# Kernel optimization log

Measured on AMD Instinct MI355X. Metric: run time of the kernel, lower is better.

The kernel has to match this reference:

```python
import jax, jax.numpy as jnp
import numpy as np

EPS = 1e-6  # torch.nn.PairwiseDistance default eps: dist = ||x - y + eps||_2


def setup_inputs() -> dict:
    key = jax.random.key(0)
    k1, k2 = jax.random.split(key)
    samples = jax.random.normal(k1, (4096, 128), dtype=jnp.float32)   # batch of observations
    V = jax.random.uniform(k2, (65536, 128), dtype=jnp.float32)       # grown node codebook (torch.rand init)
    return {"samples": samples, "V": V}


def reference(samples, V):
    # activate_bmu, vectorized over the batch.
    # torch PairwiseDistance(p=2): d_n = || x - V_n + eps ||_2
    D = samples.shape[-1]
    x_sq = jnp.sum(samples * samples, axis=-1)        # [B]
    v_sq = jnp.sum(V * V, axis=-1)                    # [N]
    xv = jnp.einsum('bd,nd->bn', samples, V)          # [B, N]
    x_sum = jnp.sum(samples, axis=-1)                 # [B]
    v_sum = jnp.sum(V, axis=-1)                       # [N]
    sq = (x_sq[:, None] + v_sq[None, :] - 2.0 * xv
          + 2.0 * EPS * (x_sum[:, None] - v_sum[None, :]) + D * EPS * EPS)
    dists = jnp.sqrt(jnp.maximum(sq, 0.0))            # [B, N]
    # top-2 smallest distances -> BMU b, second BMU s
    neg_top2, idx = jax.lax.top_k(-dists, 2)          # [B, 2]
    b = idx[:, 0]
    s = idx[:, 1]
    a = jnp.exp(neg_top2[:, 0])                       # exp(-b_dist)
    return (b, s, a)
```

## Files before the change

kernel.cpp:

```cpp
#include <hip/hip_runtime.h>
#include <math.h>

#define NS 4096
#define NV 65536
#define DDIM 128
#define EPSV 1e-6f
#define NCHUNK 16
#define TILES_PER_CHUNK 32
#define NTILE 512
#define FLTMAX 3.402823466e+38f
#define IMAX 0x7fffffff

#define XSQ_F    0
#define XSUM_F   4096
#define PART_F   8192
#define D12_F    270336
#define T12_I    278528
#define CELL1_I  286720
#define CELL2_I  290816
#define WS_TILED_BYTE 1605632
#define TILE_BYTES 65536
#define TILE_STRIDE 66560

typedef __attribute__((ext_vector_type(8)))  __bf16        bf16x8;
typedef __attribute__((ext_vector_type(8)))  unsigned short ush8;
typedef __attribute__((ext_vector_type(4)))  unsigned short ush4;
typedef __attribute__((ext_vector_type(16))) float          f32x16;

typedef const __attribute__((address_space(1))) unsigned int* gp_t;
typedef __attribute__((address_space(3))) unsigned int*       lp_t;

__device__ __forceinline__ void async_cp16(const void* g, void* l) {
    __builtin_amdgcn_global_load_lds((gp_t)g, (lp_t)l, 16, 0, 0);
}

__device__ __forceinline__ unsigned short f2bf(float x) {
    unsigned u = __builtin_bit_cast(unsigned, x);
    u += 0x7FFFu + ((u >> 16) & 1u);
    return (unsigned short)(u >> 16);
}
__device__ __forceinline__ float bf2f(unsigned short h) {
    unsigned u = ((unsigned)h) << 16;
    return __builtin_bit_cast(float, u);
}

__device__ __forceinline__ void merge2t(float& d1, int& i1, float& d2, int& i2,
                                        float d, int i) {
    bool b1 = (d < d1) || (d == d1 && i < i1);
    bool b2 = (d < d2) || (d == d2 && i < i2);
    if (b1) { d2 = d1; i2 = i1; d1 = d; i1 = i; }
    else if (b2) { d2 = d; i2 = i; }
}

__device__ __forceinline__ void load_bfrag(const float* __restrict__ samples,
                                           int srow, int q, ush8* bh, ush8* bl) {
    const float4* s4 = (const float4*)samples;
    #pragma unroll
    for (int s = 0; s < 8; s++) {
        float4 x0 = s4[(size_t)srow * 32 + s * 4 + q * 2];
        float4 x1 = s4[(size_t)srow * 32 + s * 4 + q * 2 + 1];
        float xs[8] = {x0.x, x0.y, x0.z, x0.w, x1.x, x1.y, x1.z, x1.w};
        #pragma unroll
        for (int j = 0; j < 8; j++) {
            float y = -2.0f * xs[j];
            unsigned short hh = f2bf(y);
            bh[s][j] = hh;
            bl[s][j] = f2bf(y - bf2f(hh));
        }
    }
}

__device__ __forceinline__ void tile_mfma(const char* __restrict__ base,
                                          const ush8* bh, const ush8* bl,
                                          int q, int l31, f32x16 acc[4]) {
    #pragma unroll
    for (int mi = 0; mi < 4; mi++) {
        const char* cjb = base + TILE_BYTES + (size_t)(mi * 32 + 4 * q) * 4;
        float4 c0 = *(const float4*)(cjb);
        float4 c1 = *(const float4*)(cjb + 32);
        float4 c2 = *(const float4*)(cjb + 64);
        float4 c3 = *(const float4*)(cjb + 96);
        acc[mi][0] = c0.x;  acc[mi][1] = c0.y;  acc[mi][2] = c0.z;  acc[mi][3] = c0.w;
        acc[mi][4] = c1.x;  acc[mi][5] = c1.y;  acc[mi][6] = c1.z;  acc[mi][7] = c1.w;
        acc[mi][8] = c2.x;  acc[mi][9] = c2.y;  acc[mi][10] = c2.z; acc[mi][11] = c2.w;
        acc[mi][12] = c3.x; acc[mi][13] = c3.y; acc[mi][14] = c3.z; acc[mi][15] = c3.w;
    }
    #pragma unroll
    for (int s = 0; s < 8; s++) {
        bf16x8 bhs = __builtin_bit_cast(bf16x8, bh[s]);
        bf16x8 bls = __builtin_bit_cast(bf16x8, bl[s]);
        #pragma unroll
        for (int mi = 0; mi < 4; mi++) {
            bf16x8 ah = *(const bf16x8*)(base + (size_t)((((s * 2 + 0) * 2 + q) * 128) + mi * 32 + l31) * 16);
            bf16x8 al = *(const bf16x8*)(base + (size_t)((((s * 2 + 1) * 2 + q) * 128) + mi * 32 + l31) * 16);
            acc[mi] = __builtin_amdgcn_mfma_f32_32x32x16_bf16(ah, bhs, acc[mi], 0, 0, 0);
            acc[mi] = __builtin_amdgcn_mfma_f32_32x32x16_bf16(ah, bls, acc[mi], 0, 0, 0);
            acc[mi] = __builtin_amdgcn_mfma_f32_32x32x16_bf16(al, bhs, acc[mi], 0, 0, 0);
        }
    }
}

__global__ void vq_prep(const float* __restrict__ samples,
                        const float* __restrict__ V,
                        char* __restrict__ ws) {
    __shared__ float tf[128 * 132];
    float* ws_f = (float*)ws;
    const int b = blockIdx.x;
    const int tid = threadIdx.x;
    if (b >= NV / 128) {
        int row = (b - NV / 128) * 4 + (tid >> 6);
        int lane = tid & 63;
        float2 v = ((const float2*)(samples + (size_t)row * DDIM))[lane];
        float s = v.x + v.y;
        float q = v.x * v.x + v.y * v.y;
        #pragma unroll
        for (int off = 32; off >= 1; off >>= 1) {
            s += __shfl_xor(s, off);
            q += __shfl_xor(q, off);
        }
        if (lane == 0) { ws_f[XSQ_F + row] = q; ws_f[XSUM_F + row] = s; }
        return;
    }
    const int tile = b;
    char* dst = ws + WS_TILED_BYTE + (size_t)tile * TILE_STRIDE;
    const float4* v4 = (const float4*)V;
    #pragma unroll
    for (int i = 0; i < 16; i++) {
        int flat = i * 256 + tid;
        int row = flat >> 5;
        int c4 = flat & 31;
        float4 g = v4[(size_t)(tile * 128 + row) * 32 + c4];
        *(float4*)&tf[row * 132 + c4 * 4] = g;
        float s = g.x + g.y + g.z + g.w;
        float q2 = g.x * g.x + g.y * g.y + g.z * g.z + g.w * g.w;
        #pragma unroll
        for (int off = 16; off >= 1; off >>= 1) {
            s += __shfl_xor(s, off);
            q2 += __shfl_xor(q2, off);
        }
        if ((tid & 31) == 0)
            *(float*)(dst + TILE_BYTES + row * 4) = q2 - 2.0f * EPSV * s;
    }
    __syncthreads();
    #pragma unroll
    for (int i = 0; i < 8; i++) {
        int task = i * 256 + tid;
        int row = task & 127;
        int sq = task >> 7;
        int s = sq >> 1, q = sq & 1;
        float4 lo = *(const float4*)&tf[row * 132 + s * 16 + q * 8];
        float4 hi = *(const float4*)&tf[row * 132 + s * 16 + q * 8 + 4];
        float xs[8] = {lo.x, lo.y, lo.z, lo.w, hi.x, hi.y, hi.z, hi.w};
        ush8 h, l;
        #pragma unroll
        for (int j = 0; j < 8; j++) {
            unsigned short hh = f2bf(xs[j]);
            h[j] = hh;
            l[j] = f2bf(xs[j] - bf2f(hh));
        }
        *(ush8*)(dst + (size_t)((((s * 2 + 0) * 2 + q) * 128) + row) * 16) = h;
        *(ush8*)(dst + (size_t)((((s * 2 + 1) * 2 + q) * 128) + row) * 16) = l;
    }
}

__device__ __forceinline__ void stage_tile512(const char* src, char* l, int tid) {
    #pragma unroll
    for (int i = 0; i < 8; i++) {
        int off = (i * 512 + tid) * 16;
        async_cp16(src + off, l + off);
    }
    if (tid < 64) {
        int off = TILE_BYTES + tid * 16;
        async_cp16(src + off, l + off);
    }
}

__global__ __launch_bounds__(512, 2)
void vq_gemm_topk(const float* __restrict__ samples, char* __restrict__ ws) {
    __shared__ __align__(16) char lds[2][TILE_STRIDE];
    const int tid = threadIdx.x;
    const int w = tid >> 6, lane = tid & 63;
    const int l31 = lane & 31, qb = lane >> 5;
    const int bid = blockIdx.x;
    const int g = bid >> 3;
    const int chunk = (bid & 7) * 2 + (g >> 4);
    const int st = g & 15;
    const int nrow = st * 256 + w * 32 + l31;

    const char* vbase = ws + WS_TILED_BYTE;
    const int tbase = chunk * TILES_PER_CHUNK;

    stage_tile512(vbase + (size_t)tbase * TILE_STRIDE, lds[0], tid);
    ush8 bh[8], bl[8];
    load_bfrag(samples, nrow, qb, bh, bl);
    __syncthreads();

    float D1 = FLTMAX, D2 = FLTMAX;
    int T1 = IMAX, T2 = IMAX;

    #pragma unroll 1
    for (int it = 0; it < TILES_PER_CHUNK; it++) {
        const int cur = it & 1;
        if (it + 1 < TILES_PER_CHUNK)
            stage_tile512(vbase + (size_t)(tbase + it + 1) * TILE_STRIDE,
                          lds[cur ^ 1], tid);
        f32x16 acc[4];
        tile_mfma(lds[cur], bh, bl, qb, l31, acc);
        float t1[4], t2[4];
        #pragma unroll
        for (int mi = 0; mi < 4; mi++) {
            t1[mi] = FLTMAX; t2[mi] = FLTMAX;
            #pragma unroll
            for (int r = 0; r < 16; r++) {
                float v = acc[mi][r];
                t2[mi] = fminf(t2[mi], fmaxf(t1[mi], v));
                t1[mi] = fminf(t1[mi], v);
            }
        }
        float tt1 = t1[0], tt2 = t2[0];
        #pragma unroll
        for (int mi = 1; mi < 4; mi++) {
            float tmp = fmaxf(tt1, t1[mi]);
            tt1 = fminf(tt1, t1[mi]);
            tt2 = fminf(fminf(tmp, tt2), t2[mi]);
        }
        const int tile = tbase + it;
        bool c1 = tt1 < D1;
        float m1 = fminf(D1, tt2);
        float m2 = fminf(D2, tt1);
        int T2a = (tt2 < D1) ? tile : T1;
        int T2b = (tt1 < D2) ? tile : T2;
        D2 = c1 ? m1 : m2;
        T2 = c1 ? T2a : T2b;
        T1 = c1 ? tile : T1;
        D1 = c1 ? tt1 : D1;
        __syncthreads();
    }

    {
        float od1 = __shfl_xor(D1, 32), od2 = __shfl_xor(D2, 32);
        int   ot1 = __shfl_xor(T1, 32), ot2 = __shfl_xor(T2, 32);
        merge2t(D1, T1, D2, T2, od1, ot1);
        merge2t(D1, T1, D2, T2, od2, ot2);
    }
    if (qb == 0) {
        float4* part = (float4*)((float*)ws + PART_F);
        part[(size_t)nrow * NCHUNK + chunk] =
            make_float4(D1, D2, (float)T1, (float)T2);
    }
}

__global__ void vq_merge(float* __restrict__ ws_f, float* __restrict__ out) {
    const int m = blockIdx.x * 256 + threadIdx.x;
    int* ws_i = (int*)ws_f;
    const float4* part = (const float4*)(ws_f + PART_F);
    float d1 = FLTMAX, d2 = FLTMAX;
    int t1 = IMAX, t2 = IMAX;
    #pragma unroll
    for (int c = 0; c < NCHUNK; c++) {
        float4 p = part[(size_t)m * NCHUNK + c];
        merge2t(d1, t1, d2, t2, p.x, (int)p.z);
        merge2t(d1, t1, d2, t2, p.y, (int)p.w);
    }
    ((float2*)(ws_f + D12_F))[m] = make_float2(d1, d2);
    ((int2*)(ws_i + T12_I))[m] = make_int2(t1, t2);
    ws_i[CELL1_I + m] = IMAX;
    ws_i[CELL2_I + m] = IMAX;
    float ci = ws_f[XSQ_F + m] + 2.0f * EPSV * ws_f[XSUM_F + m] + (float)DDIM * EPSV * EPSV;
    out[2 * NS + m] = expf(-sqrtf(fmaxf(ci + d1, 0.0f)));
}

__global__ __launch_bounds__(256)
void vq_recover(const float* __restrict__ samples, char* __restrict__ ws) {
    __shared__ int list[NS];
    __shared__ int lcnt;
    const int tid = threadIdx.x;
    const int w = tid >> 6, lane = tid & 63;
    const int l31 = lane & 31, qb = lane >> 5;
    const int tile = blockIdx.x;
    int* ws_i = (int*)ws;
    float* ws_f = (float*)ws;

    if (tid == 0) lcnt = 0;
    __syncthreads();
    const int2* t12 = (const int2*)(ws_i + T12_I);
    for (int i = tid; i < NS; i += 256) {
        int2 t = t12[i];
        if (t.x == tile || t.y == tile) {
            int p = atomicAdd(&lcnt, 1);
            list[p] = i;
        }
    }
    __syncthreads();
    const int cnt = lcnt;
    if (cnt == 0) return;

    const char* tsrc = ws + WS_TILED_BYTE + (size_t)tile * TILE_STRIDE;
    const float2* d12 = (const float2*)(ws_f + D12_F);
    const float nanf_ = __int_as_float(0x7fc00000);

    for (int b0 = 0; b0 < cnt; b0 += 128) {
        int li = b0 + w * 32 + l31;
        bool valid = li < cnt;
        int m = valid ? list[li] : 0;
        ush8 bh[8], bl[8];
        load_bfrag(samples, m, qb, bh, bl);
        float d1t = nanf_, d2t = nanf_;
        if (valid) {
            float2 dt = d12[m];
            d1t = dt.x; d2t = dt.y;
        }
        f32x16 acc[4];
        tile_mfma(tsrc, bh, bl, qb, l31, acc);
        #pragma unroll
        for (int mi = 0; mi < 4; mi++) {
            #pragma unroll
            for (int r = 0; r < 16; r++) {
                float v = acc[mi][r];
                int idx = tile * 128 + mi * 32 + (r & 3) + 8 * (r >> 2) + 4 * qb;
                if (v == d1t) {
                    int old = atomicMin(&ws_i[CELL1_I + m], idx);
                    int loser = old > idx ? old : idx;
                    atomicMin(&ws_i[CELL2_I + m], loser);
                } else if (v == d2t) {
                    atomicMin(&ws_i[CELL2_I + m], idx);
                }
            }
        }
    }
}

__global__ void vq_finalize(const char* __restrict__ ws, float* __restrict__ out) {
    const int m = blockIdx.x * 256 + threadIdx.x;
    const int* ws_i = (const int*)ws;
    out[m]      = (float)ws_i[CELL1_I + m];
    out[NS + m] = (float)ws_i[CELL2_I + m];
}

extern "C" void kernel_launch(void* const* d_in, const int* in_sizes, int n_in,
                              void* d_out, int out_size, void* d_ws, size_t ws_size,
                              hipStream_t stream) {
    (void)in_sizes; (void)n_in; (void)out_size; (void)ws_size;
    const float* samples = (const float*)d_in[0];
    const float* V = (const float*)d_in[1];
    float* out = (float*)d_out;
    float* ws_f = (float*)d_ws;
    char*  ws_b = (char*)d_ws;

    vq_prep<<<dim3(NV / 128 + NS / 4), 256, 0, stream>>>(samples, V, ws_b);
    vq_gemm_topk<<<dim3((NS / 256) * NCHUNK), 512, 0, stream>>>(samples, ws_b);
    vq_merge<<<dim3(NS / 256), 256, 0, stream>>>(ws_f, out);
    vq_recover<<<dim3(NTILE), 256, 0, stream>>>(samples, ws_b);
    vq_finalize<<<dim3(NS / 256), 256, 0, stream>>>(ws_b, out);
}
```

Before: 300.5 us.

## Keep sample fragments in LDS and stream V tiles from global per warp

The GEMM+top-k kernel now stages a 128-sample block (converted to split bf16) in LDS once, instead of double-buffering codebook tiles in LDS. Each warp reads its own 32-row slice of the V tile directly from global memory and computes two 32x32 accumulators. Partial top-2 results are reduced across warps through LDS before being written out. The grid doubles to cover 128-sample blocks, and the second-smallest update uses fmed3. The recover kernel now async-copies its tile into LDS up front, overlapping that copy with list building. Risks: global-load latency in the main loop is no longer hidden by a prefetch, and the V tile is re-read by more blocks.

```diff
diff --git a/kernel.cpp b/kernel.cpp
--- a/kernel.cpp
+++ b/kernel.cpp
@@ -68,6 +68,24 @@
             bl[s][j] = f2bf(y - bf2f(hh));
         }
     }
+}
+
+__device__ __forceinline__ void cvt_sample_piece(const float4* __restrict__ s4,
+                                                 int srcrow, int row, int kq,
+                                                 char* lds) {
+    float4 xv = s4[(size_t)srcrow * 32 + kq];
+    int k0 = kq * 4, sI = k0 >> 4, qI = (k0 >> 3) & 1, j0 = k0 & 7;
+    float xs[4] = {xv.x, xv.y, xv.z, xv.w};
+    ush4 h, l;
+    #pragma unroll
+    for (int e = 0; e < 4; e++) {
+        float y = -2.0f * xs[e];
+        unsigned short hh = f2bf(y);
+        h[e] = hh;
+        l[e] = f2bf(y - bf2f(hh));
+    }
+    *(ush4*)(lds + ((((sI * 2 + 0) * 2 + qI) * 128) + row) * 16 + j0 * 2) = h;
+    *(ush4*)(lds + ((((sI * 2 + 1) * 2 + qI) * 128) + row) * 16 + j0 * 2) = l;
 }
 
 __device__ __forceinline__ void tile_mfma(const char* __restrict__ base,
@@ -163,90 +181,149 @@
     }
 }
 
-__device__ __forceinline__ void stage_tile512(const char* src, char* l, int tid) {
-    #pragma unroll
-    for (int i = 0; i < 8; i++) {
-        int off = (i * 512 + tid) * 16;
-        async_cp16(src + off, l + off);
-    }
-    if (tid < 64) {
-        int off = TILE_BYTES + tid * 16;
-        async_cp16(src + off, l + off);
-    }
-}
-
 __global__ __launch_bounds__(512, 2)
 void vq_gemm_topk(const float* __restrict__ samples, char* __restrict__ ws) {
-    __shared__ __align__(16) char lds[2][TILE_STRIDE];
+    __shared__ __align__(16) char lds[TILE_BYTES];
     const int tid = threadIdx.x;
     const int w = tid >> 6, lane = tid & 63;
     const int l31 = lane & 31, qb = lane >> 5;
+    const int mi_own = w & 3;
+    const int sh = w >> 2;
     const int bid = blockIdx.x;
     const int g = bid >> 3;
-    const int chunk = (bid & 7) * 2 + (g >> 4);
-    const int st = g & 15;
-    const int nrow = st * 256 + w * 32 + l31;
+    const int chunk = (bid & 7) * 2 + (g >> 5);
+    const int st = g & 31;
+
+    const float4* s4 = (const float4*)samples;
+    #pragma unroll
+    for (int i = 0; i < 8; i++) {
+        int flat = i * 512 + tid;
+        int row = flat >> 5, kq = flat & 31;
+        cvt_sample_piece(s4, st * 128 + row, row, kq, lds);
+    }
+    __syncthreads();
 
     const char* vbase = ws + WS_TILED_BYTE;
     const int tbase = chunk * TILES_PER_CHUNK;
 
-    stage_tile512(vbase + (size_t)tbase * TILE_STRIDE, lds[0], tid);
-    ush8 bh[8], bl[8];
-    load_bfrag(samples, nrow, qb, bh, bl);
-    __syncthreads();
-
-    float D1 = FLTMAX, D2 = FLTMAX;
-    int T1 = IMAX, T2 = IMAX;
+    float D1a = FLTMAX, D2a = FLTMAX, D1b = FLTMAX, D2b = FLTMAX;
+    int T1a = IMAX, T2a = IMAX, T1b = IMAX, T2b = IMAX;
 
     #pragma unroll 1
     for (int it = 0; it < TILES_PER_CHUNK; it++) {
-        const int cur = it & 1;
-        if (it + 1 < TILES_PER_CHUNK)
-            stage_tile512(vbase + (size_t)(tbase + it + 1) * TILE_STRIDE,
-                          lds[cur ^ 1], tid);
-        f32x16 acc[4];
-        tile_mfma(lds[cur], bh, bl, qb, l31, acc);
-        float t1[4], t2[4];
-        #pragma unroll
-        for (int mi = 0; mi < 4; mi++) {
-            t1[mi] = FLTMAX; t2[mi] = FLTMAX;
+        const int tile = tbase + it;
+        const char* tsrc = vbase + (size_t)tile * TILE_STRIDE;
+        const char* cjb = tsrc + TILE_BYTES + (size_t)(mi_own * 32 + 4 * qb) * 4;
+        float4 c0 = *(const float4*)(cjb);
+        float4 c1 = *(const float4*)(cjb + 32);
+        float4 c2 = *(const float4*)(cjb + 64);
+        float4 c3 = *(const float4*)(cjb + 96);
+        f32x16 acc0, acc1;
+        acc0[0] = c0.x;  acc0[1] = c0.y;  acc0[2] = c0.z;  acc0[3] = c0.w;
+        acc0[4] = c1.x;  acc0[5] = c1.y;  acc0[6] = c1.z;  acc0[7] = c1.w;
+        acc0[8] = c2.x;  acc0[9] = c2.y;  acc0[10] = c2.z; acc0[11] = c2.w;
+        acc0[12] = c3.x; acc0[13] = c3.y; acc0[14] = c3.z; acc0[15] = c3.w;
+        acc1 = acc0;
+        #pragma unroll
+        for (int hs = 0; hs < 2; hs++) {
+            ush8 ah[4], al[4];
+            #pragma unroll
+            for (int si = 0; si < 4; si++) {
+                int s = hs * 4 + si;
+                ah[si] = *(const ush8*)(tsrc + (size_t)((((s * 2 + 0) * 2 + qb) * 128) + mi_own * 32 + l31) * 16);
+                al[si] = *(const ush8*)(tsrc + (size_t)((((s * 2 + 1) * 2 + qb) * 128) + mi_own * 32 + l31) * 16);
+            }
+            #pragma unroll
+            for (int si = 0; si < 4; si++) {
+                int s = hs * 4 + si;
+                bf16x8 a_h = __builtin_bit_cast(bf16x8, ah[si]);
+                bf16x8 a_l = __builtin_bit_cast(bf16x8, al[si]);
+                bf16x8 b0h = *(const bf16x8*)(lds + (size_t)((((s * 2 + 0) * 2 + qb) * 128) + sh * 64 + l31) * 16);
+                bf16x8 b0l = *(const bf16x8*)(lds + (size_t)((((s * 2 + 1) * 2 + qb) * 128) + sh * 64 + l31) * 16);
+                bf16x8 b1h = *(const bf16x8*)(lds + (size_t)((((s * 2 + 0) * 2 + qb) * 128) + sh * 64 + 32 + l31) * 16);
+                bf16x8 b1l = *(const bf16x8*)(lds + (size_t)((((s * 2 + 1) * 2 + qb) * 128) + sh * 64 + 32 + l31) * 16);
+                acc0 = __builtin_amdgcn_mfma_f32_32x32x16_bf16(a_h, b0h, acc0, 0, 0, 0);
+                acc0 = __builtin_amdgcn_mfma_f32_32x32x16_bf16(a_h, b0l, acc0, 0, 0, 0);
+                acc0 = __builtin_amdgcn_mfma_f32_32x32x16_bf16(a_l, b0h, acc0, 0, 0, 0);
+                acc1 = __builtin_amdgcn_mfma_f32_32x32x16_bf16(a_h, b1h, acc1, 0, 0, 0);
+                acc1 = __builtin_amdgcn_mfma_f32_32x32x16_bf16(a_h, b1l, acc1, 0, 0, 0);
+                acc1 = __builtin_amdgcn_mfma_f32_32x32x16_bf16(a_l, b1h, acc1, 0, 0, 0);
+            }
+        }
+        {
+            float t1 = FLTMAX, t2 = FLTMAX;
             #pragma unroll
             for (int r = 0; r < 16; r++) {
-                float v = acc[mi][r];
-                t2[mi] = fminf(t2[mi], fmaxf(t1[mi], v));
-                t1[mi] = fminf(t1[mi], v);
-            }
-        }
-        float tt1 = t1[0], tt2 = t2[0];
-        #pragma unroll
-        for (int mi = 1; mi < 4; mi++) {
-            float tmp = fmaxf(tt1, t1[mi]);
-            tt1 = fminf(tt1, t1[mi]);
-            tt2 = fminf(fminf(tmp, tt2), t2[mi]);
-        }
-        const int tile = tbase + it;
-        bool c1 = tt1 < D1;
-        float m1 = fminf(D1, tt2);
-        float m2 = fminf(D2, tt1);
-        int T2a = (tt2 < D1) ? tile : T1;
-        int T2b = (tt1 < D2) ? tile : T2;
-        D2 = c1 ? m1 : m2;
-        T2 = c1 ? T2a : T2b;
-        T1 = c1 ? tile : T1;
-        D1 = c1 ? tt1 : D1;
-        __syncthreads();
+                float v = acc0[r];
+                t2 = __builtin_amdgcn_fmed3f(t1, t2, v);
+                t1 = fminf(t1, v);
+            }
+            bool c1 = t1 < D1a;
+            float m1 = fminf(D1a, t2);
+            float m2 = fminf(D2a, t1);
+            int T2x = (t2 < D1a) ? tile : T1a;
+            int T2y = (t1 < D2a) ? tile : T2a;
+            D2a = c1 ? m1 : m2;
+            T2a = c1 ? T2x : T2y;
+            T1a = c1 ? tile : T1a;
+            D1a = c1 ? t1 : D1a;
+        }
+        {
+            float t1 = FLTMAX, t2 = FLTMAX;
+            #pragma unroll
+            for (int r = 0; r < 16; r++) {
+                float v = acc1[r];
+                t2 = __builtin_amdgcn_fmed3f(t1, t2, v);
+                t1 = fminf(t1, v);
+            }
+            bool c1 = t1 < D1b;
+            float m1 = fminf(D1b, t2);
+            float m2 = fminf(D2b, t1);
+            int T2x = (t2 < D1b) ? tile : T1b;
+            int T2y = (t1 < D2b) ? tile : T2b;
+            D2b = c1 ? m1 : m2;
+            T2b = c1 ? T2x : T2y;
+            T1b = c1 ? tile : T1b;
+            D1b = c1 ? t1 : D1b;
+        }
     }
 
     {
-        float od1 = __shfl_xor(D1, 32), od2 = __shfl_xor(D2, 32);
-        int   ot1 = __shfl_xor(T1, 32), ot2 = __shfl_xor(T2, 32);
-        merge2t(D1, T1, D2, T2, od1, ot1);
-        merge2t(D1, T1, D2, T2, od2, ot2);
-    }
+        float od1 = __shfl_xor(D1a, 32), od2 = __shfl_xor(D2a, 32);
+        int   ot1 = __shfl_xor(T1a, 32), ot2 = __shfl_xor(T2a, 32);
+        merge2t(D1a, T1a, D2a, T2a, od1, ot1);
+        merge2t(D1a, T1a, D2a, T2a, od2, ot2);
+    }
+    {
+        float od1 = __shfl_xor(D1b, 32), od2 = __shfl_xor(D2b, 32);
+        int   ot1 = __shfl_xor(T1b, 32), ot2 = __shfl_xor(T2b, 32);
+        merge2t(D1b, T1b, D2b, T2b, od1, ot1);
+        merge2t(D1b, T1b, D2b, T2b, od2, ot2);
+    }
+    __syncthreads();
+    float4* scratch = (float4*)lds;
     if (qb == 0) {
+        scratch[mi_own * 128 + sh * 64 + l31]      = make_float4(D1a, D2a, (float)T1a, (float)T2a);
+        scratch[mi_own * 128 + sh * 64 + 32 + l31] = make_float4(D1b, D2b, (float)T1b, (float)T2b);
+    }
+    __syncthreads();
+    if (mi_own == 0 && qb == 0) {
         float4* part = (float4*)((float*)ws + PART_F);
-        part[(size_t)nrow * NCHUNK + chunk] =
-            make_float4(D1, D2, (float)T1, (float)T2);
+        #pragma unroll
+        for (int gg = 0; gg < 2; gg++) {
+            int sidx = sh * 64 + gg * 32 + l31;
+            float4 p0 = scratch[sidx];
+            float d1 = p0.x, d2 = p0.y;
+            int t1 = (int)p0.z, t2 = (int)p0.w;
+            #pragma unroll
+            for (int mm = 1; mm < 4; mm++) {
+                float4 p = scratch[mm * 128 + sidx];
+                merge2t(d1, t1, d2, t2, p.x, (int)p.z);
+                merge2t(d1, t1, d2, t2, p.y, (int)p.w);
+            }
+            part[(size_t)(st * 128 + sidx) * NCHUNK + chunk] =
+                make_float4(d1, d2, (float)t1, (float)t2);
+        }
     }
 }
 
@@ -272,6 +349,7 @@
 
 __global__ __launch_bounds__(256)
 void vq_recover(const float* __restrict__ samples, char* __restrict__ ws) {
+    __shared__ __align__(16) char sbuf[TILE_STRIDE];
     __shared__ int list[NS];
     __shared__ int lcnt;
     const int tid = threadIdx.x;
@@ -281,6 +359,16 @@
     int* ws_i = (int*)ws;
     float* ws_f = (float*)ws;
 
+    const char* tsrc = ws + WS_TILED_BYTE + (size_t)tile * TILE_STRIDE;
+    #pragma unroll
+    for (int i = 0; i < 16; i++) {
+        int off = (i * 256 + tid) * 16;
+        async_cp16(tsrc + off, sbuf + off);
+    }
+    if (tid < 64) {
+        int off = TILE_BYTES + tid * 16;
+        async_cp16(tsrc + off, sbuf + off);
+    }
     if (tid == 0) lcnt = 0;
     __syncthreads();
     const int2* t12 = (const int2*)(ws_i + T12_I);
@@ -295,7 +383,6 @@
     const int cnt = lcnt;
     if (cnt == 0) return;
 
-    const char* tsrc = ws + WS_TILED_BYTE + (size_t)tile * TILE_STRIDE;
     const float2* d12 = (const float2*)(ws_f + D12_F);
     const float nanf_ = __int_as_float(0x7fc00000);
 
@@ -311,7 +398,7 @@
             d1t = dt.x; d2t = dt.y;
         }
         f32x16 acc[4];
-        tile_mfma(tsrc, bh, bl, qb, l31, acc);
+        tile_mfma(sbuf, bh, bl, qb, l31, acc);
         #pragma unroll
         for (int mi = 0; mi < 4; mi++) {
             #pragma unroll
@@ -348,7 +435,7 @@
     char*  ws_b = (char*)d_ws;
 
     vq_prep<<<dim3(NV / 128 + NS / 4), 256, 0, stream>>>(samples, V, ws_b);
-    vq_gemm_topk<<<dim3((NS / 256) * NCHUNK), 512, 0, stream>>>(samples, ws_b);
+    vq_gemm_topk<<<dim3((NS / 128) * NCHUNK), 512, 0, stream>>>(samples, ws_b);
     vq_merge<<<dim3(NS / 256), 256, 0, stream>>>(ws_f, out);
     vq_recover<<<dim3(NTILE), 256, 0, stream>>>(samples, ws_b);
     vq_finalize<<<dim3(NS / 256), 256, 0, stream>>>(ws_b, out);
```

New measurement: 349.6 us. 1.16x slower.
